# Kernel tuning notes

Hardware: AMD Instinct MI355X
Metric: run time of the kernel (lower is better)

## Reference

```python
import jax, jax.numpy as jnp
import numpy as np

NUM_GROUPS = 32
EPS = 1e-6


def group_norm(x, gamma, beta):
    # x: [B, C, H, W]
    b, c, h, w = x.shape
    xg = x.reshape(b, NUM_GROUPS, c // NUM_GROUPS, h, w)
    mean = xg.mean(axis=(2, 3, 4), keepdims=True)
    var = xg.var(axis=(2, 3, 4), keepdims=True)
    xn = ((xg - mean) * jax.lax.rsqrt(var + EPS)).reshape(b, c, h, w)
    return xn * gamma[None, :, None, None] + beta[None, :, None, None]


def setup_inputs() -> dict:
    key = jax.random.key(0)
    ks = jax.random.split(key, 10)
    B, C, H, W = 2, 512, 64, 64
    s = 1.0 / np.sqrt(C)
    return {
        "x": jax.random.normal(ks[0], (B, C, H, W), dtype=jnp.float32),
        "gamma": jnp.ones((C,), jnp.float32),
        "beta": jnp.zeros((C,), jnp.float32),
        "Wq": jax.random.normal(ks[1], (C, C), jnp.float32) * s,
        "bq": jnp.zeros((C,), jnp.float32),
        "Wk": jax.random.normal(ks[2], (C, C), jnp.float32) * s,
        "bk": jnp.zeros((C,), jnp.float32),
        "Wv": jax.random.normal(ks[3], (C, C), jnp.float32) * s,
        "bv": jnp.zeros((C,), jnp.float32),
        "Wo": jax.random.normal(ks[4], (C, C), jnp.float32) * s,
        "bo": jnp.zeros((C,), jnp.float32),
    }


def reference(x, gamma, beta, Wq, bq, Wk, bk, Wv, bv, Wo, bo):
    b, c, h, w = x.shape
    hn = group_norm(x, gamma, beta)               # [B,C,H,W]
    hf = hn.reshape(b, c, h * w)                  # [B,C,N]
    # 1x1 convs == channel matmuls
    q = jnp.einsum('oc,bcn->bon', Wq, hf) + bq[None, :, None]
    k = jnp.einsum('oc,bcn->bon', Wk, hf) + bk[None, :, None]
    v = jnp.einsum('oc,bcn->bon', Wv, hf) + bv[None, :, None]
    scale = float(c) ** -0.5
    scores = jnp.einsum('bci,bcj->bij', q, k) * scale   # [B,N,N]
    attn = jax.nn.softmax(scores, axis=-1)
    out = jnp.einsum('bij,bcj->bci', attn, v)            # [B,C,N]
    out = jnp.einsum('oc,bcn->bon', Wo, out) + bo[None, :, None]
    return x + out.reshape(b, c, h, w)
```

## Files before the change

kernel.cpp:

```cpp
#include <hip/hip_runtime.h>

#define BB 2
#define CC 512
#define NS 4096
#define NGROUP 32
#define TILE 128
#define BK 32
#define RSTRIDE 132

typedef __bf16 bf16_8 __attribute__((ext_vector_type(8)));
typedef __bf16 bf16_4 __attribute__((ext_vector_type(4)));
typedef float f32_4 __attribute__((ext_vector_type(4)));

__device__ __forceinline__ void gld_lds16(const __bf16* g, __bf16* l) {
  __builtin_amdgcn_global_load_lds(
      (const __attribute__((address_space(1))) unsigned int*)g,
      (__attribute__((address_space(3))) unsigned int*)l, 16, 0, 0);
}

__global__ __launch_bounds__(256) void gn_stats(const float* __restrict__ x,
                                                float* __restrict__ stats) {
  const float4* p = (const float4*)(x + (size_t)blockIdx.x * 65536);
  float s = 0.f, q = 0.f;
  for (int i = threadIdx.x; i < 16384; i += 256) {
    float4 v = p[i];
    s += v.x + v.y + v.z + v.w;
    q += v.x * v.x + v.y * v.y + v.z * v.z + v.w * v.w;
  }
#pragma unroll
  for (int off = 32; off > 0; off >>= 1) {
    s += __shfl_down(s, off, 64);
    q += __shfl_down(q, off, 64);
  }
  __shared__ float ls[4], lq[4];
  int wave = threadIdx.x >> 6, lane = threadIdx.x & 63;
  if (lane == 0) { ls[wave] = s; lq[wave] = q; }
  __syncthreads();
  if (threadIdx.x == 0) {
    float S = ls[0] + ls[1] + ls[2] + ls[3];
    float Q = lq[0] + lq[1] + lq[2] + lq[3];
    float mean = S * (1.f / 65536.f);
    float var = Q * (1.f / 65536.f) - mean * mean;
    stats[blockIdx.x * 2] = mean;
    stats[blockIdx.x * 2 + 1] = rsqrtf(var + 1e-6f);
  }
}

__global__ __launch_bounds__(256) void gn_apply_t(const float* __restrict__ x,
                                                  const float* __restrict__ stats,
                                                  const float* __restrict__ gamma,
                                                  const float* __restrict__ beta,
                                                  __bf16* __restrict__ hnT) {
  __shared__ float tile[32][33];
  int b = blockIdx.z;
  int c0 = blockIdx.y * 32;
  int n0 = blockIdx.x * 32;
  int tx = threadIdx.x;
  int ty = threadIdx.y;
  const float* xb = x + (size_t)b * CC * NS;
#pragma unroll
  for (int i = 0; i < 4; i++) {
    int c = c0 + ty + i * 8;
    float mean = stats[(b * NGROUP + (c >> 4)) * 2 + 0];
    float rstd = stats[(b * NGROUP + (c >> 4)) * 2 + 1];
    float v = xb[(size_t)c * NS + n0 + tx];
    tile[ty + i * 8][tx] = (v - mean) * rstd * gamma[c] + beta[c];
  }
  __syncthreads();
  __bf16* out = hnT + (size_t)b * NS * CC;
#pragma unroll
  for (int i = 0; i < 4; i++) {
    int n = n0 + ty + i * 8;
    out[(size_t)n * CC + c0 + tx] = (__bf16)tile[tx][ty + i * 8];
  }
}

__global__ __launch_bounds__(256) void cvt_w(const float* __restrict__ w0, const float* __restrict__ w1,
                                             const float* __restrict__ w2, const float* __restrict__ w3,
                                             __bf16* __restrict__ o0, __bf16* __restrict__ o1,
                                             __bf16* __restrict__ o2, __bf16* __restrict__ o3) {
  int tsel = blockIdx.x >> 8;
  int i = (blockIdx.x & 255) * 256 + threadIdx.x;
  const float* src = tsel == 0 ? w0 : tsel == 1 ? w1 : tsel == 2 ? w2 : w3;
  __bf16* dst = tsel == 0 ? o0 : tsel == 1 ? o1 : tsel == 2 ? o2 : o3;
  float4 v = ((const float4*)src)[i];
  bf16_4 r;
  r[0] = (__bf16)v.x; r[1] = (__bf16)v.y; r[2] = (__bf16)v.z; r[3] = (__bf16)v.w;
  ((bf16_4*)dst)[i] = r;
}

__device__ __forceinline__ void gemm_core(const __bf16* __restrict__ A, const __bf16* __restrict__ B,
                                          int K, int lda, int ldb,
                                          __bf16* lA, __bf16* lB, f32_4 (&acc)[4][2]) {
  const int t = threadIdx.x;
  const int lane = t & 63;
  const int wave = t >> 6;
  const int lrow = lane & 15, quad = lane >> 4;
  const int wrow = (wave >> 2) * 64, wcol = (wave & 3) * 32;
  const int co = (quad ^ ((lrow >> 1) & 3)) * 8;
  const int r0 = t >> 2;
  const int kp = ((t & 3) ^ ((t >> 3) & 3)) * 8;
  const __bf16* pA0 = A + (size_t)r0 * lda + kp;
  const __bf16* pB0 = B + (size_t)r0 * ldb + kp;
  for (int k0 = 0; k0 < K; k0 += BK) {
    __syncthreads();
    gld_lds16(pA0 + k0, &lA[t * 8]);
    gld_lds16(pB0 + k0, &lB[t * 8]);
    __syncthreads();
    bf16_8 af[4], bfr[2];
#pragma unroll
    for (int i = 0; i < 4; i++)
      af[i] = *(const bf16_8*)&lA[(wrow + i * 16 + lrow) * BK + co];
#pragma unroll
    for (int j = 0; j < 2; j++)
      bfr[j] = *(const bf16_8*)&lB[(wcol + j * 16 + lrow) * BK + co];
#pragma unroll
    for (int i = 0; i < 4; i++)
#pragma unroll
      for (int j = 0; j < 2; j++)
        acc[i][j] = __builtin_amdgcn_mfma_f32_16x16x32_bf16(af[i], bfr[j], acc[i][j], 0, 0, 0);
  }
}

__device__ __forceinline__ void stage_acc(float* ls, const f32_4 (&acc)[4][2], int pass) {
  const int t = threadIdx.x;
  const int lane = t & 63, wave = t >> 6;
  const int lrow = lane & 15, quad = lane >> 4;
  const int wrow = (wave >> 2) * 64, wcol = (wave & 3) * 32;
  if ((wrow >> 6) == pass) {
#pragma unroll
    for (int i = 0; i < 4; i++)
#pragma unroll
      for (int r = 0; r < 4; r++)
#pragma unroll
        for (int jj = 0; jj < 2; jj++)
          ls[(i * 16 + quad * 4 + r) * RSTRIDE + wcol + jj * 16 + lrow] = acc[i][jj][r];
  }
}

__device__ __forceinline__ void drain_bf16(const float* ls, __bf16* gdst, int ldg) {
  const int t = threadIdx.x;
#pragma unroll
  for (int k2 = 0; k2 < 4; k2++) {
    int idx = k2 * 512 + t;
    int row = idx >> 5, col = (idx & 31) * 4;
    f32_4 v = *(const f32_4*)&ls[row * RSTRIDE + col];
    bf16_4 o;
    o[0] = (__bf16)v[0]; o[1] = (__bf16)v[1]; o[2] = (__bf16)v[2]; o[3] = (__bf16)v[3];
    *(bf16_4*)&gdst[(size_t)row * ldg + col] = o;
  }
}

__device__ __forceinline__ void drain_f32(const float* ls, float* gdst, int ldg) {
  const int t = threadIdx.x;
#pragma unroll
  for (int k2 = 0; k2 < 4; k2++) {
    int idx = k2 * 512 + t;
    int row = idx >> 5, col = (idx & 31) * 4;
    f32_4 v = *(const f32_4*)&ls[row * RSTRIDE + col];
    float4 o = {v[0], v[1], v[2], v[3]};
    *(float4*)&gdst[(size_t)row * ldg + col] = o;
  }
}

__global__ __launch_bounds__(512, 4) void qkv_gemm(const __bf16* __restrict__ hnT,
                                                   const __bf16* __restrict__ Wq,
                                                   const __bf16* __restrict__ Wk,
                                                   const __bf16* __restrict__ Wv,
                                                   const float* __restrict__ bq,
                                                   const float* __restrict__ bk,
                                                   const float* __restrict__ bv,
                                                   __bf16* __restrict__ qT,
                                                   __bf16* __restrict__ kT,
                                                   __bf16* __restrict__ vv) {
  __shared__ __bf16 lA[TILE * BK];
  __shared__ __bf16 lB[TILE * BK];
  __shared__ float lsr[64 * RSTRIDE];
  const int b = blockIdx.z;
  const int id = blockIdx.x;
  const int sel = id >> 7;
  const int r = id & 127;
  const long long sBNC = (long long)NS * CC;
  const long long sBCN = (long long)CC * NS;

  int m0, n0, N;
  const __bf16 *Ap, *Bp;
  __bf16* Cp;
  const float* bias;
  if (sel < 2) {
    m0 = (r >> 2) * TILE;
    n0 = (r & 3) * TILE;
    Ap = hnT + (size_t)b * sBNC + (size_t)m0 * CC;
    Bp = (sel == 0 ? Wq : Wk) + (size_t)n0 * CC;
    Cp = (sel == 0 ? qT : kT) + (size_t)b * sBNC;
    bias = (sel == 0 ? bq : bk);
    N = CC;
  } else {
    m0 = (r & 3) * TILE;
    n0 = (r >> 2) * TILE;
    Ap = Wv + (size_t)m0 * CC;
    Bp = hnT + (size_t)b * sBNC + (size_t)n0 * CC;
    Cp = vv + (size_t)b * sBCN;
    bias = bv;
    N = NS;
  }

  f32_4 acc[4][2];
#pragma unroll
  for (int i = 0; i < 4; i++)
#pragma unroll
    for (int j = 0; j < 2; j++) acc[i][j] = {0.f, 0.f, 0.f, 0.f};

  gemm_core(Ap, Bp, CC, CC, CC, lA, lB, acc);

  const int t = threadIdx.x;
  const int lane = t & 63;
  const int lrow = lane & 15, quad = lane >> 4;
  const int wave = t >> 6;
  const int wrow = (wave >> 2) * 64, wcol = (wave & 3) * 32;
#pragma unroll
  for (int i = 0; i < 4; i++)
#pragma unroll
    for (int r2 = 0; r2 < 4; r2++) {
      float rowb = (sel == 2) ? bias[m0 + wrow + i * 16 + quad * 4 + r2] : 0.f;
#pragma unroll
      for (int j = 0; j < 2; j++) {
        float cb = (sel < 2) ? bias[n0 + wcol + j * 16 + lrow] : rowb;
        acc[i][j][r2] += cb;
      }
    }

#pragma unroll
  for (int p = 0; p < 2; p++) {
    __syncthreads();
    stage_acc(lsr, acc, p);
    __syncthreads();
    drain_bf16(lsr, Cp + (size_t)(m0 + p * 64) * N + n0, N);
  }
}

__global__ __launch_bounds__(512, 4) void e_gemm(const __bf16* __restrict__ qT,
                                                 const __bf16* __restrict__ kT,
                                                 __bf16* __restrict__ E,
                                                 float* __restrict__ l,
                                                 float scale) {
  __shared__ __bf16 lA[TILE * BK];
  __shared__ __bf16 lB[TILE * BK];
  __shared__ float lsr[64 * RSTRIDE];
  const int g = blockIdx.x;
  const int j = g & 7;
  const int b = j & 1;
  const int moct = j >> 1;
  const int k = g >> 3;
  const int sc = k >> 6;
  const int rem = k & 63;
  const int m0 = (moct * 8 + (rem >> 3)) * TILE;
  const int n0 = (sc * 8 + (rem & 7)) * TILE;
  const long long sBNC = (long long)NS * CC;
  const long long sBNN = (long long)NS * NS;
  const __bf16* Ap = qT + (size_t)b * sBNC + (size_t)m0 * CC;
  const __bf16* Bp = kT + (size_t)b * sBNC + (size_t)n0 * CC;

  f32_4 acc[4][2];
#pragma unroll
  for (int i = 0; i < 4; i++)
#pragma unroll
    for (int jj = 0; jj < 2; jj++) acc[i][jj] = {0.f, 0.f, 0.f, 0.f};

  gemm_core(Ap, Bp, CC, CC, CC, lA, lB, acc);

  const int t = threadIdx.x;
  const int lane = t & 63;
  const int lrow = lane & 15, quad = lane >> 4;
  const int wave = t >> 6;
  const int wrow = (wave >> 2) * 64, wcol = (wave & 3) * 32;
  __bf16* Ep = E + (size_t)b * sBNN;
  float* lp = l + (size_t)b * NS;

#pragma unroll
  for (int i = 0; i < 4; i++)
#pragma unroll
    for (int jj = 0; jj < 2; jj++)
#pragma unroll
      for (int r = 0; r < 4; r++)
        acc[i][jj][r] = __expf(acc[i][jj][r] * scale);

#pragma unroll
  for (int i = 0; i < 4; i++) {
#pragma unroll
    for (int r = 0; r < 4; r++) {
      int gm = m0 + wrow + i * 16 + quad * 4 + r;
      float rp = acc[i][0][r] + acc[i][1][r];
      rp += __shfl_down(rp, 8, 16);
      rp += __shfl_down(rp, 4, 16);
      rp += __shfl_down(rp, 2, 16);
      rp += __shfl_down(rp, 1, 16);
      if (lrow == 0) atomicAdd(&lp[gm], rp);
    }
  }

#pragma unroll
  for (int p = 0; p < 2; p++) {
    __syncthreads();
    stage_acc(lsr, acc, p);
    __syncthreads();
    drain_bf16(lsr, Ep + (size_t)(m0 + p * 64) * NS + n0, NS);
  }
}

__global__ __launch_bounds__(512, 4) void ao_split4(const __bf16* __restrict__ E,
                                                    const __bf16* __restrict__ vv,
                                                    __bf16* __restrict__ p0,
                                                    __bf16* __restrict__ p1,
                                                    __bf16* __restrict__ p2,
                                                    __bf16* __restrict__ p3) {
  __shared__ __bf16 lA[TILE * BK];
  __shared__ __bf16 lB[TILE * BK];
  __shared__ float lsr[64 * RSTRIDE];
  const int g = blockIdx.x;
  const int j = g & 7;
  const int b = j & 1;
  const int split = j >> 1;
  const int k = g >> 3;
  const int m0 = (k >> 2) * TILE;
  const int n0 = (k & 3) * TILE;
  const long long sBNN = (long long)NS * NS;
  const long long sBCN = (long long)CC * NS;
  const long long sBNC = (long long)NS * CC;
  const __bf16* Ap = E + (size_t)b * sBNN + (size_t)m0 * NS + (size_t)split * 1024;
  const __bf16* Bp = vv + (size_t)b * sBCN + (size_t)n0 * NS + (size_t)split * 1024;
  __bf16* Cp = (split == 0 ? p0 : split == 1 ? p1 : split == 2 ? p2 : p3) + (size_t)b * sBNC;

  f32_4 acc[4][2];
#pragma unroll
  for (int i = 0; i < 4; i++)
#pragma unroll
    for (int jj = 0; jj < 2; jj++) acc[i][jj] = {0.f, 0.f, 0.f, 0.f};

  gemm_core(Ap, Bp, 1024, NS, NS, lA, lB, acc);

#pragma unroll
  for (int p = 0; p < 2; p++) {
    __syncthreads();
    stage_acc(lsr, acc, p);
    __syncthreads();
    drain_bf16(lsr, Cp + (size_t)(m0 + p * 64) * CC + n0, CC);
  }
}

__global__ __launch_bounds__(256) void reduce_ao4(const __bf16* __restrict__ p0,
                                                  const __bf16* __restrict__ p1,
                                                  const __bf16* __restrict__ p2,
                                                  const __bf16* __restrict__ p3,
                                                  const float* __restrict__ l,
                                                  __bf16* __restrict__ o) {
  int i = blockIdx.x * 256 + threadIdx.x;
  int row = i >> 6;
  float inv = 1.f / l[row];
  bf16_8 a = ((const bf16_8*)p0)[i];
  bf16_8 c = ((const bf16_8*)p1)[i];
  bf16_8 d = ((const bf16_8*)p2)[i];
  bf16_8 e = ((const bf16_8*)p3)[i];
  bf16_8 r;
#pragma unroll
  for (int k = 0; k < 8; k++)
    r[k] = (__bf16)(((float)a[k] + (float)c[k] + (float)d[k] + (float)e[k]) * inv);
  ((bf16_8*)o)[i] = r;
}

__global__ __launch_bounds__(512, 4) void wo_split(const __bf16* __restrict__ Wo,
                                                   const __bf16* __restrict__ aoT,
                                                   float* __restrict__ pw0,
                                                   float* __restrict__ pw1) {
  __shared__ __bf16 lA[TILE * BK];
  __shared__ __bf16 lB[TILE * BK];
  __shared__ float lsr[64 * RSTRIDE];
  const int b = blockIdx.z & 1;
  const int split = blockIdx.z >> 1;
  const int m0 = blockIdx.y * TILE;
  const int n0 = blockIdx.x * TILE;
  const long long sBNC = (long long)NS * CC;
  const long long sBCN = (long long)CC * NS;
  const __bf16* Ap = Wo + (size_t)m0 * CC + (size_t)split * 256;
  const __bf16* Bp = aoT + (size_t)b * sBNC + (size_t)n0 * CC + (size_t)split * 256;
  float* Cp = (split ? pw1 : pw0) + (size_t)b * sBCN;

  f32_4 acc[4][2];
#pragma unroll
  for (int i = 0; i < 4; i++)
#pragma unroll
    for (int j = 0; j < 2; j++) acc[i][j] = {0.f, 0.f, 0.f, 0.f};

  gemm_core(Ap, Bp, 256, CC, CC, lA, lB, acc);

#pragma unroll
  for (int p = 0; p < 2; p++) {
    __syncthreads();
    stage_acc(lsr, acc, p);
    __syncthreads();
    drain_f32(lsr, Cp + (size_t)(m0 + p * 64) * NS + n0, NS);
  }
}

__global__ __launch_bounds__(256) void final_out(const float* __restrict__ pw0,
                                                 const float* __restrict__ pw1,
                                                 const float* __restrict__ bo,
                                                 const float* __restrict__ x,
                                                 float* __restrict__ out) {
  int i = blockIdx.x * 256 + threadIdx.x;
  int o = (i >> 10) & (CC - 1);
  float bias = bo[o];
  float4 a = ((const float4*)pw0)[i];
  float4 c = ((const float4*)pw1)[i];
  float4 xr = ((const float4*)x)[i];
  float4 r;
  r.x = a.x + c.x + bias + xr.x;
  r.y = a.y + c.y + bias + xr.y;
  r.z = a.z + c.z + bias + xr.z;
  r.w = a.w + c.w + bias + xr.w;
  ((float4*)out)[i] = r;
}

extern "C" void kernel_launch(void* const* d_in, const int* in_sizes, int n_in,
                              void* d_out, int out_size, void* d_ws, size_t ws_size,
                              hipStream_t stream) {
  const float* x = (const float*)d_in[0];
  const float* gamma = (const float*)d_in[1];
  const float* beta = (const float*)d_in[2];
  const float* Wq = (const float*)d_in[3];
  const float* bq = (const float*)d_in[4];
  const float* Wk = (const float*)d_in[5];
  const float* bk = (const float*)d_in[6];
  const float* Wv = (const float*)d_in[7];
  const float* bv = (const float*)d_in[8];
  const float* Wo = (const float*)d_in[9];
  const float* bo = (const float*)d_in[10];
  float* out = (float*)d_out;

  char* ws = (char*)d_ws;
  __bf16* hnT = (__bf16*)(ws + 0);
  __bf16* qT  = (__bf16*)(ws + 8388608);
  __bf16* kT  = (__bf16*)(ws + 16777216);
  __bf16* vv  = (__bf16*)(ws + 25165824);
  __bf16* aoT = (__bf16*)(ws + 33554432);
  __bf16* Eb  = (__bf16*)(ws + 41943040);
  float* pw0  = (float*)(ws + 41943040);
  float* pw1  = (float*)(ws + 58720256);
  __bf16* Wqb = (__bf16*)(ws + 109051904);
  __bf16* Wkb = (__bf16*)(ws + 109576192);
  __bf16* Wvb = (__bf16*)(ws + 110100480);
  __bf16* Wob = (__bf16*)(ws + 110624768);
  float* stats = (float*)(ws + 111149056);
  float* lsum = (float*)(ws + 109051904);
  __bf16* p0 = hnT;
  __bf16* p1 = qT;
  __bf16* p2 = kT;
  __bf16* p3 = aoT;

  const float scale = 0.044194173824159216f;

  cvt_w<<<1024, 256, 0, stream>>>(Wq, Wk, Wv, Wo, Wqb, Wkb, Wvb, Wob);
  gn_stats<<<BB * NGROUP, 256, 0, stream>>>(x, stats);
  gn_apply_t<<<dim3(NS / 32, CC / 32, BB), dim3(32, 8), 0, stream>>>(x, stats, gamma, beta, hnT);

  qkv_gemm<<<dim3(384, 1, BB), 512, 0, stream>>>(hnT, Wqb, Wkb, Wvb, bq, bk, bv, qT, kT, vv);

  hipMemsetAsync(lsum, 0, BB * NS * sizeof(float), stream);
  e_gemm<<<2048, 512, 0, stream>>>(qT, kT, Eb, lsum, scale);

  ao_split4<<<1024, 512, 0, stream>>>(Eb, vv, p0, p1, p2, p3);
  reduce_ao4<<<2048, 256, 0, stream>>>(p0, p1, p2, p3, lsum, aoT);

  wo_split<<<dim3(NS / TILE, CC / TILE, 2 * BB), 512, 0, stream>>>(Wob, aoT, pw0, pw1);
  final_out<<<4096, 256, 0, stream>>>(pw0, pw1, bo, x, out);
}
```

Before: 273.5 us.

## Double GEMM K-step to 64, alias LDS buffers, write E directly

The shared GEMM core now loads two 32-wide K slices per barrier pair, so each k-loop iteration does twice the MFMA work and the number of __syncthreads halves. LDS is unioned: the A/B tiles and the epilogue staging buffer share one allocation, which keeps per-block LDS near 33 KB despite the larger tiles. In e_gemm the LDS-staged drain is removed and exp values are stored to E straight from registers as scattered bf16 writes. That drops two barriers and the staging pass, but the per-element stores are less coalesced than the vectorized drain.

```diff
diff --git a/kernel.cpp b/kernel.cpp
--- a/kernel.cpp
+++ b/kernel.cpp
@@ -5,12 +5,13 @@
 #define NS 4096
 #define NGROUP 32
 #define TILE 128
-#define BK 32
 #define RSTRIDE 132
 
 typedef __bf16 bf16_8 __attribute__((ext_vector_type(8)));
 typedef __bf16 bf16_4 __attribute__((ext_vector_type(4)));
 typedef float f32_4 __attribute__((ext_vector_type(4)));
+
+#define SMEM_BYTES 33792
 
 __device__ __forceinline__ void gld_lds16(const __bf16* g, __bf16* l) {
   __builtin_amdgcn_global_load_lds(
@@ -100,25 +101,32 @@
   const int co = (quad ^ ((lrow >> 1) & 3)) * 8;
   const int r0 = t >> 2;
   const int kp = ((t & 3) ^ ((t >> 3) & 3)) * 8;
-  const __bf16* pA0 = A + (size_t)r0 * lda + kp;
-  const __bf16* pB0 = B + (size_t)r0 * ldb + kp;
-  for (int k0 = 0; k0 < K; k0 += BK) {
-    __syncthreads();
-    gld_lds16(pA0 + k0, &lA[t * 8]);
-    gld_lds16(pB0 + k0, &lB[t * 8]);
-    __syncthreads();
-    bf16_8 af[4], bfr[2];
-#pragma unroll
-    for (int i = 0; i < 4; i++)
-      af[i] = *(const bf16_8*)&lA[(wrow + i * 16 + lrow) * BK + co];
-#pragma unroll
-    for (int j = 0; j < 2; j++)
-      bfr[j] = *(const bf16_8*)&lB[(wcol + j * 16 + lrow) * BK + co];
-#pragma unroll
-    for (int i = 0; i < 4; i++)
+  const __bf16* pA = A + (size_t)r0 * lda + kp;
+  const __bf16* pB = B + (size_t)r0 * ldb + kp;
+  for (int k0 = 0; k0 < K; k0 += 64) {
+    __syncthreads();
+    gld_lds16(pA + k0,      &lA[t * 8]);
+    gld_lds16(pA + k0 + 32, &lA[4096 + t * 8]);
+    gld_lds16(pB + k0,      &lB[t * 8]);
+    gld_lds16(pB + k0 + 32, &lB[4096 + t * 8]);
+    __syncthreads();
+#pragma unroll
+    for (int ks = 0; ks < 2; ks++) {
+      const __bf16* la = lA + ks * 4096;
+      const __bf16* lb = lB + ks * 4096;
+      bf16_8 af[4], bfr[2];
+#pragma unroll
+      for (int i = 0; i < 4; i++)
+        af[i] = *(const bf16_8*)&la[(wrow + i * 16 + lrow) * 32 + co];
 #pragma unroll
       for (int j = 0; j < 2; j++)
-        acc[i][j] = __builtin_amdgcn_mfma_f32_16x16x32_bf16(af[i], bfr[j], acc[i][j], 0, 0, 0);
+        bfr[j] = *(const bf16_8*)&lb[(wcol + j * 16 + lrow) * 32 + co];
+#pragma unroll
+      for (int i = 0; i < 4; i++)
+#pragma unroll
+        for (int j = 0; j < 2; j++)
+          acc[i][j] = __builtin_amdgcn_mfma_f32_16x16x32_bf16(af[i], bfr[j], acc[i][j], 0, 0, 0);
+    }
   }
 }
 
@@ -173,9 +181,10 @@
                                                    __bf16* __restrict__ qT,
                                                    __bf16* __restrict__ kT,
                                                    __bf16* __restrict__ vv) {
-  __shared__ __bf16 lA[TILE * BK];
-  __shared__ __bf16 lB[TILE * BK];
-  __shared__ float lsr[64 * RSTRIDE];
+  __shared__ char smem[SMEM_BYTES];
+  __bf16* lA = (__bf16*)smem;
+  __bf16* lB = (__bf16*)(smem + 16384);
+  float* lsr = (float*)smem;
   const int b = blockIdx.z;
   const int id = blockIdx.x;
   const int sel = id >> 7;
@@ -244,9 +253,9 @@
                                                  __bf16* __restrict__ E,
                                                  float* __restrict__ l,
                                                  float scale) {
-  __shared__ __bf16 lA[TILE * BK];
-  __shared__ __bf16 lB[TILE * BK];
-  __shared__ float lsr[64 * RSTRIDE];
+  __shared__ char smem[32768];
+  __bf16* lA = (__bf16*)smem;
+  __bf16* lB = (__bf16*)(smem + 16384);
   const int g = blockIdx.x;
   const int j = g & 7;
   const int b = j & 1;
@@ -276,21 +285,19 @@
   const int wrow = (wave >> 2) * 64, wcol = (wave & 3) * 32;
   __bf16* Ep = E + (size_t)b * sBNN;
   float* lp = l + (size_t)b * NS;
-
-#pragma unroll
-  for (int i = 0; i < 4; i++)
-#pragma unroll
-    for (int jj = 0; jj < 2; jj++)
-#pragma unroll
-      for (int r = 0; r < 4; r++)
-        acc[i][jj][r] = __expf(acc[i][jj][r] * scale);
-
 #pragma unroll
   for (int i = 0; i < 4; i++) {
 #pragma unroll
     for (int r = 0; r < 4; r++) {
       int gm = m0 + wrow + i * 16 + quad * 4 + r;
-      float rp = acc[i][0][r] + acc[i][1][r];
+      float rp = 0.f;
+#pragma unroll
+      for (int jj = 0; jj < 2; jj++) {
+        int gn = n0 + wcol + jj * 16 + lrow;
+        float ev = __expf(acc[i][jj][r] * scale);
+        rp += ev;
+        Ep[(size_t)gm * NS + gn] = (__bf16)ev;
+      }
       rp += __shfl_down(rp, 8, 16);
       rp += __shfl_down(rp, 4, 16);
       rp += __shfl_down(rp, 2, 16);
@@ -298,14 +305,6 @@
       if (lrow == 0) atomicAdd(&lp[gm], rp);
     }
   }
-
-#pragma unroll
-  for (int p = 0; p < 2; p++) {
-    __syncthreads();
-    stage_acc(lsr, acc, p);
-    __syncthreads();
-    drain_bf16(lsr, Ep + (size_t)(m0 + p * 64) * NS + n0, NS);
-  }
 }
 
 __global__ __launch_bounds__(512, 4) void ao_split4(const __bf16* __restrict__ E,
@@ -314,9 +313,10 @@
                                                     __bf16* __restrict__ p1,
                                                     __bf16* __restrict__ p2,
                                                     __bf16* __restrict__ p3) {
-  __shared__ __bf16 lA[TILE * BK];
-  __shared__ __bf16 lB[TILE * BK];
-  __shared__ float lsr[64 * RSTRIDE];
+  __shared__ char smem[SMEM_BYTES];
+  __bf16* lA = (__bf16*)smem;
+  __bf16* lB = (__bf16*)(smem + 16384);
+  float* lsr = (float*)smem;
   const int g = blockIdx.x;
   const int j = g & 7;
   const int b = j & 1;
@@ -372,9 +372,10 @@
                                                    const __bf16* __restrict__ aoT,
                                                    float* __restrict__ pw0,
                                                    float* __restrict__ pw1) {
-  __shared__ __bf16 lA[TILE * BK];
-  __shared__ __bf16 lB[TILE * BK];
-  __shared__ float lsr[64 * RSTRIDE];
+  __shared__ char smem[SMEM_BYTES];
+  __bf16* lA = (__bf16*)smem;
+  __bf16* lB = (__bf16*)(smem + 16384);
+  float* lsr = (float*)smem;
   const int b = blockIdx.z & 1;
   const int split = blockIdx.z >> 1;
   const int m0 = blockIdx.y * TILE;
```

Measured after the change: 252.2 us. -7.8%, faster.
